# Kernel tuning notes

Hardware: AMD Instinct MI355X
Metric: run time of the kernel (lower is better)

The kernel has to match this reference:

```python
import jax, jax.numpy as jnp
import numpy as np

N_SUBWORDS = 8192
N_WORDS = 6000
HIDDEN = 1024


def setup_inputs() -> dict:
    key = jax.random.key(0)
    k_h, k_s, k_w = jax.random.split(key, 3)
    hidden_states = jax.random.normal(k_h, (N_SUBWORDS, HIDDEN), dtype=jnp.float32)
    # sorted start indices of words; ends are inclusive and contiguous up to the next start
    word_starts = jnp.sort(jax.random.randint(k_s, (N_WORDS,), 0, N_SUBWORDS, dtype=jnp.int64))
    nxt = jnp.concatenate([word_starts[1:], jnp.array([N_SUBWORDS], dtype=jnp.int64)])
    word_ends = jnp.maximum(nxt - 1, word_starts)  # inclusive ends, >= starts
    # params of self.subword_attn = Linear(hidden_size, 1)
    w_attn = jax.random.normal(k_w, (HIDDEN, 1), dtype=jnp.float32) * 0.02
    b_attn = jnp.zeros((1,), dtype=jnp.float32)
    return {
        "hidden_states": hidden_states,
        "word_starts": word_starts,
        "word_ends": word_ends,
        "w_attn": w_attn,
        "b_attn": b_attn,
    }


def reference(hidden_states, word_starts, word_ends, w_attn, b_attn):
    """Word-encoder masked attention pooling (wl-coref _wordencoder_attn_scores + pooling).

    hidden_states: [n_subwords, hidden]
    word_starts/word_ends: [n_words] inclusive span boundaries over subwords
    Returns pooled word embeddings: [n_words, hidden]
    """
    n_sub = hidden_states.shape[0]
    pos = jnp.arange(n_sub)  # [n_subwords]
    # torch: (arange >= starts) * (arange < ends+1)  -> inclusive end mask
    mask = (pos[None, :] >= word_starts[:, None]) & (pos[None, :] <= word_ends[:, None])
    # per-subword scalar score: Linear(hidden, 1), broadcast to [n_words, n_subwords]
    scores = (hidden_states @ w_attn + b_attn).T  # [1, n_subwords]
    # torch adds log(mask.float()) == -inf outside span; scores are finite
    logits = jnp.where(mask, scores, -jnp.inf)
    attn = jax.nn.softmax(logits, axis=1)  # [n_words, n_subwords]
    # pool subword embeddings into word embeddings
    return attn @ hidden_states  # [n_words, hidden]
```

## Files before the change

### kernel.cpp

```cpp
#include <hip/hip_runtime.h>
#include <hip/hip_bf16.h>
#include <math.h>

#define N_SUBWORDS 8192
#define N_WORDS    6000
#define HIDDEN     1024

__global__ __launch_bounds__(256) void coref_fused_kernel(
    const float* __restrict__ hs,
    const int*   __restrict__ starts,
    const int*   __restrict__ ends,
    const float* __restrict__ w_attn,
    const float* __restrict__ b_attn,
    float*       __restrict__ out)
{
    __shared__ float red[8];

    const int w    = blockIdx.x;
    const int tid  = threadIdx.x;
    const int lane = tid & 63;
    const int wid  = tid >> 6;

    const int s0 = starts[w];
    const int s1 = ends[w];

    const float4 wv = ((const float4*)w_attn)[tid];
    const float  b  = b_attn[0];

    float  m = 0.f, l = 1.f;
    float4 acc = make_float4(0.f, 0.f, 0.f, 0.f);

    for (int s = s0; s <= s1; ++s) {
        float4 h = ((const float4*)(hs + (size_t)s * HIDDEN))[tid];

        float part = h.x * wv.x + h.y * wv.y + h.z * wv.z + h.w * wv.w;
        #pragma unroll
        for (int off = 32; off > 0; off >>= 1)
            part += __shfl_down(part, off, 64);

        const int slot = ((s - s0) & 1) << 2;
        if (lane == 0) red[slot + wid] = part;
        __syncthreads();
        const float score =
            red[slot + 0] + red[slot + 1] + red[slot + 2] + red[slot + 3] + b;

        if (s == s0) {
            m = score;
            l = 1.f;
            acc = h;
        } else {
            const float mn    = fmaxf(m, score);
            const float alpha = __expf(m - mn);
            const float p     = __expf(score - mn);
            m = mn;
            l = l * alpha + p;
            acc.x = acc.x * alpha + p * h.x;
            acc.y = acc.y * alpha + p * h.y;
            acc.z = acc.z * alpha + p * h.z;
            acc.w = acc.w * alpha + p * h.w;
        }
    }

    const float inv_l = 1.f / l;
    float4 o;
    o.x = acc.x * inv_l;
    o.y = acc.y * inv_l;
    o.z = acc.z * inv_l;
    o.w = acc.w * inv_l;
    ((float4*)(out + (size_t)w * HIDDEN))[tid] = o;
}

extern "C" void kernel_launch(void* const* d_in, const int* in_sizes, int n_in,
                              void* d_out, int out_size, void* d_ws, size_t ws_size,
                              hipStream_t stream) {
    const float* hs     = (const float*)d_in[0];
    const int*   starts = (const int*)d_in[1];
    const int*   ends   = (const int*)d_in[2];
    const float* w_attn = (const float*)d_in[3];
    const float* b_attn = (const float*)d_in[4];
    float*       out    = (float*)d_out;

    coref_fused_kernel<<<dim3(N_WORDS), dim3(256), 0, stream>>>(
        hs, starts, ends, w_attn, b_attn, out);
}
```

Before: 92.66 us.

## Assign one wavefront per word and drop block-level barrier reduction

Each 64-lane wavefront now handles a whole word: every lane loads four float4 chunks of each subword row and reduces the score with xor shuffles inside the wave. This removes the shared-memory write and __syncthreads needed for every subword in the per-block design. Blocks now cover four words, so each block runs fewer barriers. In exchange each thread holds more registers and has more loads in flight, and the wavefronts in a block can do unequal work because word spans differ in length.

```diff
diff --git a/kernel.cpp b/kernel.cpp
--- a/kernel.cpp
+++ b/kernel.cpp
@@ -6,7 +6,7 @@
 #define N_WORDS    6000
 #define HIDDEN     1024
 
-__global__ __launch_bounds__(256) void coref_fused_kernel(
+__global__ __launch_bounds__(256) void coref_fused_wave_kernel(
     const float* __restrict__ hs,
     const int*   __restrict__ starts,
     const int*   __restrict__ ends,
@@ -14,60 +14,76 @@
     const float* __restrict__ b_attn,
     float*       __restrict__ out)
 {
-    __shared__ float red[8];
-
-    const int w    = blockIdx.x;
     const int tid  = threadIdx.x;
     const int lane = tid & 63;
-    const int wid  = tid >> 6;
+    const int w    = blockIdx.x * 4 + (tid >> 6);
+    if (w >= N_WORDS) return;
 
     const int s0 = starts[w];
     const int s1 = ends[w];
 
-    const float4 wv = ((const float4*)w_attn)[tid];
-    const float  b  = b_attn[0];
+    const float4* __restrict__ wvp = (const float4*)w_attn;
+    float4 wv[4];
+#pragma unroll
+    for (int j = 0; j < 4; ++j)
+        wv[j] = wvp[lane + 64 * j];
+    const float b = b_attn[0];
 
     float  m = 0.f, l = 1.f;
-    float4 acc = make_float4(0.f, 0.f, 0.f, 0.f);
+    float4 acc[4];
 
     for (int s = s0; s <= s1; ++s) {
-        float4 h = ((const float4*)(hs + (size_t)s * HIDDEN))[tid];
+        const float4* __restrict__ row = (const float4*)(hs + (size_t)s * HIDDEN);
+        float4 h[4];
+#pragma unroll
+        for (int j = 0; j < 4; ++j)
+            h[j] = row[lane + 64 * j];
 
-        float part = h.x * wv.x + h.y * wv.y + h.z * wv.z + h.w * wv.w;
-        #pragma unroll
+        float part = 0.f;
+#pragma unroll
+        for (int j = 0; j < 4; ++j)
+            part += h[j].x * wv[j].x + h[j].y * wv[j].y +
+                    h[j].z * wv[j].z + h[j].w * wv[j].w;
+
+#pragma unroll
         for (int off = 32; off > 0; off >>= 1)
-            part += __shfl_down(part, off, 64);
+            part += __shfl_xor(part, off, 64);
 
-        const int slot = ((s - s0) & 1) << 2;
-        if (lane == 0) red[slot + wid] = part;
-        __syncthreads();
-        const float score =
-            red[slot + 0] + red[slot + 1] + red[slot + 2] + red[slot + 3] + b;
+        const float score = part + b;
 
         if (s == s0) {
             m = score;
             l = 1.f;
-            acc = h;
+#pragma unroll
+            for (int j = 0; j < 4; ++j)
+                acc[j] = h[j];
         } else {
             const float mn    = fmaxf(m, score);
             const float alpha = __expf(m - mn);
             const float p     = __expf(score - mn);
             m = mn;
             l = l * alpha + p;
-            acc.x = acc.x * alpha + p * h.x;
-            acc.y = acc.y * alpha + p * h.y;
-            acc.z = acc.z * alpha + p * h.z;
-            acc.w = acc.w * alpha + p * h.w;
+#pragma unroll
+            for (int j = 0; j < 4; ++j) {
+                acc[j].x = acc[j].x * alpha + p * h[j].x;
+                acc[j].y = acc[j].y * alpha + p * h[j].y;
+                acc[j].z = acc[j].z * alpha + p * h[j].z;
+                acc[j].w = acc[j].w * alpha + p * h[j].w;
+            }
         }
     }
 
     const float inv_l = 1.f / l;
-    float4 o;
-    o.x = acc.x * inv_l;
-    o.y = acc.y * inv_l;
-    o.z = acc.z * inv_l;
-    o.w = acc.w * inv_l;
-    ((float4*)(out + (size_t)w * HIDDEN))[tid] = o;
+    float4* __restrict__ orow = (float4*)(out + (size_t)w * HIDDEN);
+#pragma unroll
+    for (int j = 0; j < 4; ++j) {
+        float4 o;
+        o.x = acc[j].x * inv_l;
+        o.y = acc[j].y * inv_l;
+        o.z = acc[j].z * inv_l;
+        o.w = acc[j].w * inv_l;
+        orow[lane + 64 * j] = o;
+    }
 }
 
 extern "C" void kernel_launch(void* const* d_in, const int* in_sizes, int n_in,
@@ -80,6 +96,6 @@
     const float* b_attn = (const float*)d_in[4];
     float*       out    = (float*)d_out;
 
-    coref_fused_kernel<<<dim3(N_WORDS), dim3(256), 0, stream>>>(
+    coref_fused_wave_kernel<<<dim3((N_WORDS + 3) / 4), dim3(256), 0, stream>>>(
         hs, starts, ends, w_attn, b_attn, out);
 }
```

Result: faster. 89.57 us (-3.3%).
